# Optimization experiments

Measured on AMD Instinct MI355X. Metric: run time of the kernel, lower is better.

The kernel has to match this reference:

```python
import jax, jax.numpy as jnp
import numpy as np

B, T, E, H = 4, 1024, 1024, 16
D = E // H  # head_dim = 64


def setup_inputs() -> dict:
    key = jax.random.key(0)
    ks = jax.random.split(key, 6)
    s = 0.02  # realistic init scale for stable softmax
    return {
        "hidden_states": jax.random.normal(ks[0], (B, T, E), jnp.float32),
        "attention_mask": jnp.zeros((B, 1, T, T), jnp.float32),
        "Wq": jax.random.normal(ks[1], (E, E), jnp.float32) * s,
        "bq": jnp.zeros((E,), jnp.float32),
        "Wk": jax.random.normal(ks[2], (E, E), jnp.float32) * s,
        "bk": jnp.zeros((E,), jnp.float32),
        "Wv": jax.random.normal(ks[3], (E, E), jnp.float32) * s,
        "bv": jnp.zeros((E,), jnp.float32),
        "Wo": jax.random.normal(ks[4], (E, E), jnp.float32) * s,
        "bo": jnp.zeros((E,), jnp.float32),
    }


def reference(hidden_states, attention_mask, Wq, bq, Wk, bk, Wv, bv, Wo, bo):
    b, t, e = hidden_states.shape
    scaling = jnp.asarray(D, hidden_states.dtype) ** -0.5
    # q_proj weights/bias are pre-scaled in the module; equivalent to scaling q output
    q = (hidden_states @ Wq.T + bq) * scaling      # [B,T,E]
    k = hidden_states @ Wk.T + bk                   # self-attention path (no cache)
    v = hidden_states @ Wv.T + bv
    q = q.reshape(b, t, H, D)
    k = k.reshape(b, t, H, D)
    v = v.reshape(b, t, H, D)
    # bmm(q, k^T): [B,H,T,S] score matrix (materialized, as in the original)
    scores = jnp.einsum("bthd,bshd->bhts", q, k) + attention_mask
    probs = jax.nn.softmax(scores, axis=-1)
    ctx = jnp.einsum("bhts,bshd->bthd", probs, v).reshape(b, t, e)
    return ctx @ Wo.T + bo
```

## Files before the change

### kernel.cpp

```cpp
#include <hip/hip_runtime.h>
#include <math.h>

#define BB 4
#define TT 1024
#define EE 1024
#define HH 16
#define DD 64
#define KDIM 1024
#define N_HS (4096 * 1024)
#define N_W  (1024 * 1024)
#define NQKV (BB * HH * TT * DD)
#define NMASK (BB * TT * TT)

typedef _Float16 f16x8 __attribute__((ext_vector_type(8)));
typedef float    f32x4 __attribute__((ext_vector_type(4)));

__device__ __forceinline__ unsigned short f2h(float x) {
    _Float16 h = (_Float16)x;
    return __builtin_bit_cast(unsigned short, h);
}
__device__ __forceinline__ void split_h(float x, unsigned short& hi, unsigned short& lo) {
    _Float16 h = (_Float16)x;
    hi = __builtin_bit_cast(unsigned short, h);
    lo = f2h(x - (float)h);
}

__device__ __forceinline__ void gload16(const void* g, void* l) {
    __builtin_amdgcn_global_load_lds(
        (const __attribute__((address_space(1))) void*)g,
        (__attribute__((address_space(3))) void*)l, 16, 0, 0);
}

__global__ __launch_bounds__(256)
void split_kernel(const float* __restrict__ hs,
                  const float* __restrict__ Wq, const float* __restrict__ Wk,
                  const float* __restrict__ Wv, const float* __restrict__ Wo,
                  const float* __restrict__ maskp,
                  unsigned short* __restrict__ ws,
                  unsigned short* __restrict__ maskh)
{
    const int u = blockIdx.x * 256 + threadIdx.x;
    const float* src;
    unsigned short* dst;
    if (u < (N_HS / 4)) {
        src = hs + (size_t)u * 4;
        dst = ws + (size_t)u * 4;
    } else if (u < (N_HS / 4) + N_W) {
        int v = u - N_HS / 4;
        int wsel = v >> 18;
        int wo   = v & 0x3FFFF;
        const float* Wsrc = (wsel == 0) ? Wq : (wsel == 1) ? Wk : (wsel == 2) ? Wv : Wo;
        src = Wsrc + (size_t)wo * 4;
        dst = ws + (size_t)N_HS + (size_t)wsel * N_W + (size_t)wo * 4;
    } else {
        int v = u - (N_HS / 4) - N_W;
        src = maskp + (size_t)v * 4;
        dst = maskh + (size_t)v * 4;
    }
    float4 x = *(const float4*)src;
    ushort4 h4;
    h4.x = f2h(x.x); h4.y = f2h(x.y); h4.z = f2h(x.z); h4.w = f2h(x.w);
    *(ushort4*)dst = h4;
}

__global__ __launch_bounds__(256)
void qkv_kernel(const unsigned short* __restrict__ hsp,
                const unsigned short* __restrict__ wqp,
                const float* __restrict__ bq, const float* __restrict__ bk,
                const float* __restrict__ bv,
                unsigned short* __restrict__ qkvb)
{
    __shared__ unsigned short Ah[128 * 32], Bh[128 * 32];

    const int widx  = blockIdx.x >> 3;
    const int nbase = (blockIdx.x & 7) * 128;
    const int mbase = blockIdx.y * 128;
    const unsigned short* Wp = wqp + (size_t)widx * N_W;
    const float* bias = (widx == 0) ? bq : (widx == 1) ? bk : bv;
    const float scale = (widx == 0) ? 0.125f : 1.0f;

    const int tid  = threadIdx.x;
    const int w    = tid >> 6;
    const int lane = tid & 63;
    const int quad = lane >> 4;
    const int l16  = lane & 15;
    const int wm   = (w >> 1) * 64;
    const int wn   = (w & 1) * 64;

    f32x4 acc[4][4];
#pragma unroll
    for (int i = 0; i < 4; i++)
#pragma unroll
        for (int j = 0; j < 4; j++) acc[i][j] = (f32x4)0.f;

#pragma unroll 1
    for (int kt = 0; kt < KDIM; kt += 32) {
        __syncthreads();
#pragma unroll
        for (int i = 0; i < 2; i++) {
            int u = tid + i * 256;
            int r = u >> 2, c = u & 3;
            int q = c ^ ((r >> 1) & 3);
            gload16(hsp + (size_t)(mbase + r) * KDIM + kt + q * 8, &Ah[u * 8]);
            gload16(Wp  + (size_t)(nbase + r) * KDIM + kt + q * 8, &Bh[u * 8]);
        }
        __syncthreads();

        f16x8 af[4], bfr[4];
#pragma unroll
        for (int i = 0; i < 4; i++) {
            int r = wm + i * 16 + l16;
            af[i] = *(const f16x8*)&Ah[(r * 4 + (quad ^ ((r >> 1) & 3))) * 8];
        }
#pragma unroll
        for (int j = 0; j < 4; j++) {
            int r = wn + j * 16 + l16;
            bfr[j] = *(const f16x8*)&Bh[(r * 4 + (quad ^ ((r >> 1) & 3))) * 8];
        }
#pragma unroll
        for (int i = 0; i < 4; i++)
#pragma unroll
            for (int j = 0; j < 4; j++)
                acc[i][j] = __builtin_amdgcn_mfma_f32_16x16x32_f16(af[i], bfr[j], acc[i][j], 0, 0, 0);
    }

    if (widx == 2) {
        unsigned short* vtp = qkvb + 2 * (size_t)NQKV;
#pragma unroll
        for (int j = 0; j < 4; j++) {
            int n = nbase + wn + j * 16 + l16;
            int h = n >> 6, d = n & 63;
            float bj = bias[n];
#pragma unroll
            for (int i = 0; i < 4; i++) {
                int m = mbase + wm + i * 16 + quad * 4;
                int b = m >> 10, t0 = m & 1023;
                ushort4 pk;
                pk.x = f2h(acc[i][j][0] + bj);
                pk.y = f2h(acc[i][j][1] + bj);
                pk.z = f2h(acc[i][j][2] + bj);
                pk.w = f2h(acc[i][j][3] + bj);
                *(ushort4*)(vtp + ((size_t)(b * HH + h) * DD + d) * TT + t0) = pk;
            }
        }
    } else {
        unsigned short* dst = qkvb + (size_t)widx * NQKV;
#pragma unroll
        for (int j = 0; j < 4; j++) {
            int n = nbase + wn + j * 16 + l16;
            int h = n >> 6, d = n & 63;
            float bj = bias[n];
#pragma unroll
            for (int i = 0; i < 4; i++)
#pragma unroll
                for (int rr = 0; rr < 4; rr++) {
                    int m = mbase + wm + i * 16 + quad * 4 + rr;
                    int b = m >> 10, t = m & 1023;
                    dst[(((size_t)(b * HH + h) * TT + t) * DD + d)] =
                        f2h((acc[i][j][rr] + bj) * scale);
                }
        }
    }
}

__global__ __launch_bounds__(256)
void outproj_kernel(const unsigned short* __restrict__ ctxh,
                    const unsigned short* __restrict__ ctxl,
                    const unsigned short* __restrict__ wop,
                    const float* __restrict__ bo, float* __restrict__ out)
{
    __shared__ unsigned short Ach[64 * 32], Acl[64 * 32], Bh[128 * 32];

    const int nbase = blockIdx.x * 128;
    const int mbase = blockIdx.y * 64;

    const int tid  = threadIdx.x;
    const int w    = tid >> 6;
    const int lane = tid & 63;
    const int quad = lane >> 4;
    const int l16  = lane & 15;
    const int wm   = (w >> 1) * 32;
    const int wn   = (w & 1) * 64;

    f32x4 acc[2][4];
#pragma unroll
    for (int i = 0; i < 2; i++)
#pragma unroll
        for (int j = 0; j < 4; j++) acc[i][j] = (f32x4)0.f;

#pragma unroll 1
    for (int kt = 0; kt < KDIM; kt += 32) {
        __syncthreads();
        {
            int r = tid >> 2, c = tid & 3;
            int q = c ^ ((r >> 1) & 3);
            size_t ga = (size_t)(mbase + r) * KDIM + kt + q * 8;
            gload16(ctxh + ga, &Ach[tid * 8]);
            gload16(ctxl + ga, &Acl[tid * 8]);
        }
#pragma unroll
        for (int i = 0; i < 2; i++) {
            int u = tid + i * 256;
            int r = u >> 2, c = u & 3;
            int q = c ^ ((r >> 1) & 3);
            gload16(wop + (size_t)(nbase + r) * KDIM + kt + q * 8, &Bh[u * 8]);
        }
        __syncthreads();

        f16x8 ah[2], al[2], bfr[4];
#pragma unroll
        for (int i = 0; i < 2; i++) {
            int r = wm + i * 16 + l16;
            int slot = (r * 4 + (quad ^ ((r >> 1) & 3))) * 8;
            ah[i] = *(const f16x8*)&Ach[slot];
            al[i] = *(const f16x8*)&Acl[slot];
        }
#pragma unroll
        for (int j = 0; j < 4; j++) {
            int r = wn + j * 16 + l16;
            bfr[j] = *(const f16x8*)&Bh[(r * 4 + (quad ^ ((r >> 1) & 3))) * 8];
        }
#pragma unroll
        for (int i = 0; i < 2; i++)
#pragma unroll
            for (int j = 0; j < 4; j++) {
                acc[i][j] = __builtin_amdgcn_mfma_f32_16x16x32_f16(ah[i], bfr[j], acc[i][j], 0, 0, 0);
                acc[i][j] = __builtin_amdgcn_mfma_f32_16x16x32_f16(al[i], bfr[j], acc[i][j], 0, 0, 0);
            }
    }

#pragma unroll
    for (int j = 0; j < 4; j++) {
        int n = nbase + wn + j * 16 + l16;
        float bj = bo[n];
#pragma unroll
        for (int i = 0; i < 2; i++)
#pragma unroll
            for (int rr = 0; rr < 4; rr++) {
                int m = mbase + wm + i * 16 + quad * 4 + rr;
                out[(size_t)m * EE + n] = acc[i][j][rr] + bj;
            }
    }
}

__global__ __launch_bounds__(256)
void attn_kernel(const unsigned short* __restrict__ qp_, const unsigned short* __restrict__ kp_,
                 const unsigned short* __restrict__ vtp_,
                 const unsigned short* __restrict__ maskh,
                 unsigned short* __restrict__ ctxh, unsigned short* __restrict__ ctxl)
{
    __shared__ unsigned short Ks[2][64 * 64];
    __shared__ unsigned short Vt[2][64 * 64];
    __shared__ unsigned short Ps[64 * 64];

    const int bh = blockIdx.y;
    const int b  = bh >> 4;
    const int h  = bh & 15;
    const int m0 = blockIdx.x * 64;
    const size_t hoff = (size_t)bh * TT * DD;
    const unsigned short* qhp = qp_ + hoff;
    const unsigned short* khp = kp_ + hoff;
    const unsigned short* vtp = vtp_ + hoff;
    const _Float16* mb = (const _Float16*)(maskh + (size_t)b * TT * TT);

    const int tid  = threadIdx.x;
    const int w    = tid >> 6;
    const int lane = tid & 63;
    const int quad = lane >> 4;
    const int l16  = lane & 15;

    auto stage = [&](int n0s, int bb) {
#pragma unroll
        for (int i = 0; i < 2; i++) {
            int u = tid + i * 256;
            int r = u >> 3, cp = u & 7;
            int c = cp ^ (r & 7);
            gload16(khp + (size_t)(n0s + r) * DD + c * 8, &Ks[bb][u * 8]);
            gload16(vtp + (size_t)r * TT + n0s + c * 8,   &Vt[bb][u * 8]);
        }
    };

    f16x8 qf[2];
#pragma unroll
    for (int s = 0; s < 2; s++)
        qf[s] = *(const f16x8*)(qhp + (size_t)(m0 + w * 16 + l16) * DD + s * 32 + quad * 8);

    f32x4 o[4];
    float m_i[4], l_i[4];
#pragma unroll
    for (int t = 0; t < 4; t++) o[t] = (f32x4)0.f;
#pragma unroll
    for (int r = 0; r < 4; r++) { m_i[r] = -INFINITY; l_i[r] = 0.f; }

    stage(0, 0);

#pragma unroll 1
    for (int it = 0; it < TT / 64; it++) {
        const int n0  = it * 64;
        const int cur = it & 1;

        __syncthreads();
        if (it + 1 < TT / 64) stage(n0 + 64, 1 - cur);

        _Float16 mreg[4][4];
#pragma unroll
        for (int t = 0; t < 4; t++)
#pragma unroll
            for (int r = 0; r < 4; r++)
                mreg[t][r] = mb[(size_t)(m0 + w * 16 + quad * 4 + r) * TT + n0 + 16 * t + l16];

        f32x4 st[4];
#pragma unroll
        for (int t = 0; t < 4; t++) st[t] = (f32x4)0.f;
#pragma unroll
        for (int s = 0; s < 2; s++)
#pragma unroll
            for (int t = 0; t < 4; t++) {
                int R = 16 * t + l16;
                const f16x8 kf = *(const f16x8*)&Ks[cur][(R * 8 + ((s * 4 + quad) ^ (R & 7))) * 8];
                st[t] = __builtin_amdgcn_mfma_f32_16x16x32_f16(qf[s], kf, st[t], 0, 0, 0);
            }
#pragma unroll
        for (int t = 0; t < 4; t++)
#pragma unroll
            for (int r = 0; r < 4; r++)
                st[t][r] += (float)mreg[t][r];

        float rm[4], rs[4], alpha[4];
#pragma unroll
        for (int r = 0; r < 4; r++)
            rm[r] = fmaxf(fmaxf(st[0][r], st[1][r]), fmaxf(st[2][r], st[3][r]));
#pragma unroll
        for (int mky = 1; mky < 16; mky <<= 1)
#pragma unroll
            for (int r = 0; r < 4; r++)
                rm[r] = fmaxf(rm[r], __shfl_xor(rm[r], mky));
#pragma unroll
        for (int r = 0; r < 4; r++) {
            float mn = fmaxf(m_i[r], rm[r]);
            alpha[r] = __expf(m_i[r] - mn);
            m_i[r]   = mn;
            rs[r]    = 0.f;
        }
#pragma unroll
        for (int t = 0; t < 4; t++)
#pragma unroll
            for (int r = 0; r < 4; r++) {
                float p = __expf(st[t][r] - m_i[r]);
                st[t][r] = p;
                rs[r] += p;
            }
#pragma unroll
        for (int mky = 1; mky < 16; mky <<= 1)
#pragma unroll
            for (int r = 0; r < 4; r++)
                rs[r] += __shfl_xor(rs[r], mky);
#pragma unroll
        for (int r = 0; r < 4; r++)
            l_i[r] = l_i[r] * alpha[r] + rs[r];
#pragma unroll
        for (int t = 0; t < 4; t++)
#pragma unroll
            for (int r = 0; r < 4; r++)
                o[t][r] *= alpha[r];

#pragma unroll
        for (int t = 0; t < 4; t++)
#pragma unroll
            for (int r = 0; r < 4; r++) {
                int R = w * 16 + quad * 4 + r;
                int j = 16 * t + l16;
                Ps[R * 64 + (((j >> 3) ^ (R & 7)) * 8) + (j & 7)] = f2h(st[t][r]);
            }

#pragma unroll
        for (int s = 0; s < 2; s++) {
            int Rr = w * 16 + l16;
            const f16x8 pf = *(const f16x8*)&Ps[Rr * 64 + (((s * 4 + quad) ^ (Rr & 7)) * 8)];
#pragma unroll
            for (int t = 0; t < 4; t++) {
                int R = 16 * t + l16;
                const f16x8 vf = *(const f16x8*)&Vt[cur][(R * 8 + ((s * 4 + quad) ^ (R & 7))) * 8];
                o[t] = __builtin_amdgcn_mfma_f32_16x16x32_f16(pf, vf, o[t], 0, 0, 0);
            }
        }
    }

#pragma unroll
    for (int r = 0; r < 4; r++) {
        float inv = 1.0f / l_i[r];
        int m = m0 + w * 16 + quad * 4 + r;
#pragma unroll
        for (int t = 0; t < 4; t++) {
            float val = o[t][r] * inv;
            unsigned short hi, lo;
            split_h(val, hi, lo);
            size_t off = (size_t)(b * TT + m) * EE + h * DD + 16 * t + l16;
            ctxh[off] = hi;
            ctxl[off] = lo;
        }
    }
}

extern "C" void kernel_launch(void* const* d_in, const int* in_sizes, int n_in,
                              void* d_out, int out_size, void* d_ws, size_t ws_size,
                              hipStream_t stream)
{
    const float* hs   = (const float*)d_in[0];
    const float* mask = (const float*)d_in[1];
    const float* Wq   = (const float*)d_in[2];
    const float* bq   = (const float*)d_in[3];
    const float* Wk   = (const float*)d_in[4];
    const float* bk   = (const float*)d_in[5];
    const float* Wv   = (const float*)d_in[6];
    const float* bv   = (const float*)d_in[7];
    const float* Wo   = (const float*)d_in[8];
    const float* bo   = (const float*)d_in[9];
    float* out = (float*)d_out;

    unsigned short* ws    = (unsigned short*)d_ws;
    unsigned short* hsp   = ws;
    unsigned short* wqp   = ws + (size_t)N_HS;
    unsigned short* wop   = wqp + 3 * (size_t)N_W;
    unsigned short* qkvb  = wqp + 4 * (size_t)N_W;
    unsigned short* qp    = qkvb;
    unsigned short* kp    = qp + (size_t)NQKV;
    unsigned short* vtp   = kp + (size_t)NQKV;
    unsigned short* ctxl  = vtp + (size_t)NQKV;
    unsigned short* maskh = ctxl + (size_t)N_HS;
    unsigned short* ctxh  = ws;

    split_kernel<<<12288, 256, 0, stream>>>(hs, Wq, Wk, Wv, Wo, mask, ws, maskh);
    qkv_kernel<<<dim3(24, 32), 256, 0, stream>>>(hsp, wqp, bq, bk, bv, qkvb);
    attn_kernel<<<dim3(TT / 64, BB * HH), 256, 0, stream>>>(qp, kp, vtp, maskh, ctxh, ctxl);
    outproj_kernel<<<dim3(8, 64), 256, 0, stream>>>(ctxh, ctxl, wop, bo, out);
}
```

Baseline: 252.9 us.

## Shrink attention blocks to 32 rows, reorder grid, compute row sums via MFMA

The attention kernel now uses 128-thread blocks covering 32 query rows. The grid puts batch·head on the x dimension, so blocks sharing K/V run close together, which is meant to raise occupancy and L2 reuse. The double-buffered K/V staging is replaced by a single buffer with two barriers per tile, which gives up load/compute overlap. The running max is now shared by the four rows each lane holds, and the softmax denominator is accumulated with an extra MFMA against a ones vector instead of shuffle reductions. The shared max could underflow if rows in a group have very different scores.

```diff
diff --git a/kernel.cpp b/kernel.cpp
--- a/kernel.cpp
+++ b/kernel.cpp
@@ -243,20 +243,20 @@
     }
 }
 
-__global__ __launch_bounds__(256)
+__global__ __launch_bounds__(128)
 void attn_kernel(const unsigned short* __restrict__ qp_, const unsigned short* __restrict__ kp_,
                  const unsigned short* __restrict__ vtp_,
                  const unsigned short* __restrict__ maskh,
                  unsigned short* __restrict__ ctxh, unsigned short* __restrict__ ctxl)
 {
-    __shared__ unsigned short Ks[2][64 * 64];
-    __shared__ unsigned short Vt[2][64 * 64];
-    __shared__ unsigned short Ps[64 * 64];
-
-    const int bh = blockIdx.y;
+    __shared__ unsigned short Ks[64 * 64];
+    __shared__ unsigned short Vt[64 * 64];
+    __shared__ unsigned short Ps[32 * 64];
+
+    const int bh = blockIdx.x;
     const int b  = bh >> 4;
     const int h  = bh & 15;
-    const int m0 = blockIdx.x * 64;
+    const int m0 = blockIdx.y * 32;
     const size_t hoff = (size_t)bh * TT * DD;
     const unsigned short* qhp = qp_ + hoff;
     const unsigned short* khp = kp_ + hoff;
@@ -269,45 +269,39 @@
     const int quad = lane >> 4;
     const int l16  = lane & 15;
 
-    auto stage = [&](int n0s, int bb) {
-#pragma unroll
-        for (int i = 0; i < 2; i++) {
-            int u = tid + i * 256;
+    f16x8 ones;
+#pragma unroll
+    for (int j = 0; j < 8; j++) ones[j] = (_Float16)1.0f;
+
+    f16x8 qf[2];
+#pragma unroll
+    for (int s = 0; s < 2; s++)
+        qf[s] = *(const f16x8*)(qhp + (size_t)(m0 + w * 16 + l16) * DD + s * 32 + quad * 8);
+
+    f32x4 o[4], lacc = (f32x4)0.f;
+    float m_q = -INFINITY;
+#pragma unroll
+    for (int t = 0; t < 4; t++) o[t] = (f32x4)0.f;
+
+#pragma unroll 1
+    for (int n0 = 0; n0 < TT; n0 += 64) {
+        _Float16 mreg[4][4];
+#pragma unroll
+        for (int t = 0; t < 4; t++)
+#pragma unroll
+            for (int r = 0; r < 4; r++)
+                mreg[t][r] = mb[(size_t)(m0 + w * 16 + quad * 4 + r) * TT + n0 + 16 * t + l16];
+
+        __syncthreads();
+#pragma unroll
+        for (int i = 0; i < 4; i++) {
+            int u = tid + i * 128;
             int r = u >> 3, cp = u & 7;
             int c = cp ^ (r & 7);
-            gload16(khp + (size_t)(n0s + r) * DD + c * 8, &Ks[bb][u * 8]);
-            gload16(vtp + (size_t)r * TT + n0s + c * 8,   &Vt[bb][u * 8]);
-        }
-    };
-
-    f16x8 qf[2];
-#pragma unroll
-    for (int s = 0; s < 2; s++)
-        qf[s] = *(const f16x8*)(qhp + (size_t)(m0 + w * 16 + l16) * DD + s * 32 + quad * 8);
-
-    f32x4 o[4];
-    float m_i[4], l_i[4];
-#pragma unroll
-    for (int t = 0; t < 4; t++) o[t] = (f32x4)0.f;
-#pragma unroll
-    for (int r = 0; r < 4; r++) { m_i[r] = -INFINITY; l_i[r] = 0.f; }
-
-    stage(0, 0);
-
-#pragma unroll 1
-    for (int it = 0; it < TT / 64; it++) {
-        const int n0  = it * 64;
-        const int cur = it & 1;
-
-        __syncthreads();
-        if (it + 1 < TT / 64) stage(n0 + 64, 1 - cur);
-
-        _Float16 mreg[4][4];
-#pragma unroll
-        for (int t = 0; t < 4; t++)
-#pragma unroll
-            for (int r = 0; r < 4; r++)
-                mreg[t][r] = mb[(size_t)(m0 + w * 16 + quad * 4 + r) * TT + n0 + 16 * t + l16];
+            gload16(khp + (size_t)(n0 + r) * DD + c * 8, &Ks[u * 8]);
+            gload16(vtp + (size_t)r * TT + n0 + c * 8,   &Vt[u * 8]);
+        }
+        __syncthreads();
 
         f32x4 st[4];
 #pragma unroll
@@ -317,7 +311,7 @@
 #pragma unroll
             for (int t = 0; t < 4; t++) {
                 int R = 16 * t + l16;
-                const f16x8 kf = *(const f16x8*)&Ks[cur][(R * 8 + ((s * 4 + quad) ^ (R & 7))) * 8];
+                const f16x8 kf = *(const f16x8*)&Ks[(R * 8 + ((s * 4 + quad) ^ (R & 7))) * 8];
                 st[t] = __builtin_amdgcn_mfma_f32_16x16x32_f16(qf[s], kf, st[t], 0, 0, 0);
             }
 #pragma unroll
@@ -326,43 +320,29 @@
             for (int r = 0; r < 4; r++)
                 st[t][r] += (float)mreg[t][r];
 
-        float rm[4], rs[4], alpha[4];
-#pragma unroll
-        for (int r = 0; r < 4; r++)
-            rm[r] = fmaxf(fmaxf(st[0][r], st[1][r]), fmaxf(st[2][r], st[3][r]));
+        float rm = st[0][0];
+#pragma unroll
+        for (int t = 0; t < 4; t++)
+#pragma unroll
+            for (int r = 0; r < 4; r++) rm = fmaxf(rm, st[t][r]);
 #pragma unroll
         for (int mky = 1; mky < 16; mky <<= 1)
+            rm = fmaxf(rm, __shfl_xor(rm, mky));
+        float mnew  = fmaxf(m_q, rm);
+        float alpha = __expf(m_q - mnew);
+        m_q = mnew;
+
+#pragma unroll
+        for (int t = 0; t < 4; t++)
 #pragma unroll
             for (int r = 0; r < 4; r++)
-                rm[r] = fmaxf(rm[r], __shfl_xor(rm[r], mky));
-#pragma unroll
-        for (int r = 0; r < 4; r++) {
-            float mn = fmaxf(m_i[r], rm[r]);
-            alpha[r] = __expf(m_i[r] - mn);
-            m_i[r]   = mn;
-            rs[r]    = 0.f;
-        }
-#pragma unroll
-        for (int t = 0; t < 4; t++)
-#pragma unroll
-            for (int r = 0; r < 4; r++) {
-                float p = __expf(st[t][r] - m_i[r]);
-                st[t][r] = p;
-                rs[r] += p;
-            }
-#pragma unroll
-        for (int mky = 1; mky < 16; mky <<= 1)
+                st[t][r] = __expf(st[t][r] - m_q);
+#pragma unroll
+        for (int t = 0; t < 4; t++)
 #pragma unroll
             for (int r = 0; r < 4; r++)
-                rs[r] += __shfl_xor(rs[r], mky);
-#pragma unroll
-        for (int r = 0; r < 4; r++)
-            l_i[r] = l_i[r] * alpha[r] + rs[r];
-#pragma unroll
-        for (int t = 0; t < 4; t++)
-#pragma unroll
-            for (int r = 0; r < 4; r++)
-                o[t][r] *= alpha[r];
+                o[t][r] *= alpha;
+        lacc *= alpha;
 
 #pragma unroll
         for (int t = 0; t < 4; t++)
@@ -377,10 +357,11 @@
         for (int s = 0; s < 2; s++) {
             int Rr = w * 16 + l16;
             const f16x8 pf = *(const f16x8*)&Ps[Rr * 64 + (((s * 4 + quad) ^ (Rr & 7)) * 8)];
+            lacc = __builtin_amdgcn_mfma_f32_16x16x32_f16(pf, ones, lacc, 0, 0, 0);
 #pragma unroll
             for (int t = 0; t < 4; t++) {
                 int R = 16 * t + l16;
-                const f16x8 vf = *(const f16x8*)&Vt[cur][(R * 8 + ((s * 4 + quad) ^ (R & 7))) * 8];
+                const f16x8 vf = *(const f16x8*)&Vt[(R * 8 + ((s * 4 + quad) ^ (R & 7))) * 8];
                 o[t] = __builtin_amdgcn_mfma_f32_16x16x32_f16(pf, vf, o[t], 0, 0, 0);
             }
         }
@@ -388,7 +369,7 @@
 
 #pragma unroll
     for (int r = 0; r < 4; r++) {
-        float inv = 1.0f / l_i[r];
+        float inv = 1.0f / lacc[r];
         int m = m0 + w * 16 + quad * 4 + r;
 #pragma unroll
         for (int t = 0; t < 4; t++) {
@@ -432,6 +413,6 @@
 
     split_kernel<<<12288, 256, 0, stream>>>(hs, Wq, Wk, Wv, Wo, mask, ws, maskh);
     qkv_kernel<<<dim3(24, 32), 256, 0, stream>>>(hsp, wqp, bq, bk, bv, qkvb);
-    attn_kernel<<<dim3(TT / 64, BB * HH), 256, 0, stream>>>(qp, kp, vtp, maskh, ctxh, ctxl);
+    attn_kernel<<<dim3(BB * HH, TT / 32), 128, 0, stream>>>(qp, kp, vtp, maskh, ctxh, ctxl);
     outproj_kernel<<<dim3(8, 64), 256, 0, stream>>>(ctxh, ctxl, wop, bo, out);
 }
```

Result: faster. 244.3 us (-3.4%).
